# Kernel optimization log

Measured on AMD Instinct MI355X. Metric: run time of the kernel, lower is better.

Reference implementation:

```python
import jax, jax.numpy as jnp
import numpy as np

N = 50000      # nodes
E = 800000     # edges (avg degree 16)
D = 128        # extended_lat_size = latent_size(124) + 4
G = 256        # number of graphs in the batch
H = 8 * D      # 1024, hidden width of MLP stack


def _w(k, shape):
    return jax.random.normal(k, shape, jnp.float32) * 0.02


def setup_inputs() -> dict:
    key = jax.random.key(0)
    ks = jax.random.split(key, 20)
    x = jax.random.normal(ks[0], (N, D), jnp.float32)
    edge_index = jax.random.randint(ks[1], (2, E), 0, N, dtype=jnp.int32)
    batch_vector = jnp.sort(jax.random.randint(ks[2], (N,), 0, G, dtype=jnp.int32))
    return {
        "x": x,
        "edge_index": edge_index,
        "batch_vector": batch_vector,
        # GCNConv layers
        "W1": _w(ks[3], (D, 2 * D)), "b1": jnp.zeros((2 * D,), jnp.float32),
        "W2": _w(ks[4], (2 * D, D)), "b2": jnp.zeros((D,), jnp.float32),
        # lazy Linear stack (in-dims resolved from dataflow)
        "Wl1": _w(ks[5], (D, D)),   "bl1": jnp.zeros((D,), jnp.float32),
        "Wl2": _w(ks[6], (D, H)),   "bl2": jnp.zeros((H,), jnp.float32),
        "Wl22": _w(ks[7], (H, H)),  "bl22": jnp.zeros((H,), jnp.float32),
        "Wl23": _w(ks[8], (H, H)),  "bl23": jnp.zeros((H,), jnp.float32),
        "Wl3": _w(ks[9], (H, D)),   "bl3": jnp.zeros((D,), jnp.float32),
    }


def gcn_conv(x, W, b, row, col):
    """PyG GCNConv: linear transform, add self-loops, symmetric norm, scatter-add."""
    h = x @ W  # [N, F_out]
    n = x.shape[0]
    loop = jnp.arange(n, dtype=row.dtype)
    r = jnp.concatenate([row, loop])   # source nodes
    c = jnp.concatenate([col, loop])   # target nodes
    deg = jax.ops.segment_sum(jnp.ones_like(c, dtype=h.dtype), c, num_segments=n)
    dinv = jnp.where(deg > 0, jax.lax.rsqrt(deg), 0.0)
    norm = dinv[r] * dinv[c]                         # [E+N]
    msg = h[r] * norm[:, None]                       # gather + scale
    out = jax.ops.segment_sum(msg, c, num_segments=n)  # scatter-add
    return out + b


def global_mean_pool(x, batch, num_graphs):
    s = jax.ops.segment_sum(x, batch, num_segments=num_graphs)
    cnt = jax.ops.segment_sum(jnp.ones((x.shape[0],), x.dtype), batch, num_segments=num_graphs)
    return s / jnp.maximum(cnt, 1.0)[:, None]


def reference(x, edge_index, batch_vector, W1, b1, W2, b2,
              Wl1, bl1, Wl2, bl2, Wl22, bl22, Wl23, bl23, Wl3, bl3):
    row, col = edge_index[0], edge_index[1]
    h = jax.nn.relu(gcn_conv(x, W1, b1, row, col))
    h = jax.nn.relu(gcn_conv(h, W2, b2, row, col))
    g = global_mean_pool(h, batch_vector, G)         # [G, D]
    g = jax.nn.relu(g @ Wl1 + bl1)
    g = jax.nn.relu(g @ Wl2 + bl2)
    g = jax.nn.relu(g @ Wl22 + bl22)
    g = jax.nn.relu(g @ Wl23 + bl23)
    g = g @ Wl3 + bl3                                 # [G, D]
    return jnp.squeeze(g).reshape(-1)                 # flatten -> [G*D]
```

## Files before the change

kernel.cpp:

```cpp
#include <hip/hip_runtime.h>


typedef __attribute__((ext_vector_type(8))) short bf16x8;
typedef __attribute__((ext_vector_type(8))) ushort u16x8;
typedef __attribute__((ext_vector_type(4))) float f32x4;

#define ADJ_STRIDE 64

__device__ __forceinline__ ushort f2bf(float f) {
    unsigned u = __float_as_uint(f);
    unsigned r = (u + 0x7FFFu + ((u >> 16) & 1u)) >> 16;
    return (ushort)r;
}
__device__ __forceinline__ float bf2f(ushort h) {
    return __uint_as_float(((unsigned)h) << 16);
}
__device__ __forceinline__ float bflo(unsigned u) {
    return __uint_as_float(u << 16);
}
__device__ __forceinline__ float bfhi(unsigned u) {
    return __uint_as_float(u & 0xffff0000u);
}
__device__ __forceinline__ float idinv(int d) {
    return rsqrtf((float)(d + 1));
}
__device__ __forceinline__ void gload16(const ushort* g, ushort* l) {
    __builtin_amdgcn_global_load_lds(
        (const __attribute__((address_space(1))) void*)g,
        (__attribute__((address_space(3))) void*)l, 16, 0, 0);
}

#define SWZ(r) (((r) >> 1) & 3)

struct PreArgs {
    const int* row;
    const int* col;
    int E, N;
    int* indeg;
    int* adjf;
    const float* W[7];
    ushort* Th[7];
    ushort* Tl[7];
    int K[7], Nn[7], off[8];
    const float* x;
    ushort* xb;
    int total8;
    int nFill, nT;
};

__global__ __launch_bounds__(256) void preproc_mega_kernel(PreArgs a) {
    __shared__ float sm[64][65];
    int bid = blockIdx.x;
    int tid = threadIdx.x;

    if (bid < a.nFill) {
        int r = bid & 7, chunk = bid >> 3;
        int lo = (int)(((long long)a.N * r) >> 3);
        int hi = (int)(((long long)a.N * (r + 1)) >> 3);
        int E4 = a.E >> 2;
#pragma unroll
        for (int v = 0; v < 2; ++v) {
            int i = chunk * 512 + v * 256 + tid;
            if (i < E4) {
                int c0 = __builtin_nontemporal_load(a.col + i * 4 + 0);
                int c1 = __builtin_nontemporal_load(a.col + i * 4 + 1);
                int c2 = __builtin_nontemporal_load(a.col + i * 4 + 2);
                int c3 = __builtin_nontemporal_load(a.col + i * 4 + 3);
                int r0 = __builtin_nontemporal_load(a.row + i * 4 + 0);
                int r1 = __builtin_nontemporal_load(a.row + i * 4 + 1);
                int r2 = __builtin_nontemporal_load(a.row + i * 4 + 2);
                int r3 = __builtin_nontemporal_load(a.row + i * 4 + 3);
                if (c0 >= lo && c0 < hi) {
                    int p = atomicAdd(&a.indeg[c0], 1);
                    if (p < ADJ_STRIDE) a.adjf[(c0 << 6) + p] = r0;
                }
                if (c1 >= lo && c1 < hi) {
                    int p = atomicAdd(&a.indeg[c1], 1);
                    if (p < ADJ_STRIDE) a.adjf[(c1 << 6) + p] = r1;
                }
                if (c2 >= lo && c2 < hi) {
                    int p = atomicAdd(&a.indeg[c2], 1);
                    if (p < ADJ_STRIDE) a.adjf[(c2 << 6) + p] = r2;
                }
                if (c3 >= lo && c3 < hi) {
                    int p = atomicAdd(&a.indeg[c3], 1);
                    if (p < ADJ_STRIDE) a.adjf[(c3 << 6) + p] = r3;
                }
            }
        }
        if (bid == 0 && tid < (a.E & 3)) {
            int e = (a.E & ~3) + tid;
            int c = a.col[e];
            int p = atomicAdd(&a.indeg[c], 1);
            if (p < ADJ_STRIDE) a.adjf[(c << 6) + p] = a.row[e];
        }
        return;
    }

    if (bid < a.nFill + a.nT) {
        int b = bid - a.nFill;
        int j = 0;
#pragma unroll
        for (int t = 1; t < 7; ++t) if (b >= a.off[t]) j = t;
        int local = b - a.off[j];
        int K = a.K[j], Nn = a.Nn[j];
        int kt = K >> 6;
        int k0 = (local % kt) * 64, n0 = (local / kt) * 64;
        const float* W = a.W[j];
        ushort* Th = a.Th[j];
        ushort* Tl = a.Tl[j];

        int r = tid >> 2, cq = tid & 3;
#pragma unroll
        for (int i = 0; i < 4; ++i) {
            float4 v = *(const float4*)(W + (size_t)(k0 + r) * Nn + n0 + cq * 16 + i * 4);
            sm[r][cq * 16 + i * 4 + 0] = v.x;
            sm[r][cq * 16 + i * 4 + 1] = v.y;
            sm[r][cq * 16 + i * 4 + 2] = v.z;
            sm[r][cq * 16 + i * 4 + 3] = v.w;
        }
        __syncthreads();
        int n = tid >> 2, kq = tid & 3;
        ushort h[16], l[16];
#pragma unroll
        for (int i = 0; i < 16; ++i) {
            float v = sm[kq * 16 + i][n];
            h[i] = f2bf(v);
            l[i] = f2bf(v - bf2f(h[i]));
        }
        size_t o = (size_t)(n0 + n) * K + k0 + kq * 16;
        *(u16x8*)(&Th[o]) = *(u16x8*)&h[0];
        *(u16x8*)(&Th[o + 8]) = *(u16x8*)&h[8];
        *(u16x8*)(&Tl[o]) = *(u16x8*)&l[0];
        *(u16x8*)(&Tl[o + 8]) = *(u16x8*)&l[8];
        return;
    }

    {
        int idx = (bid - a.nFill - a.nT) * 256 + tid;
        if (idx >= a.total8) return;
        const float4* xp = (const float4*)a.x;
        float4 v0 = xp[idx * 2], v1 = xp[idx * 2 + 1];
        ushort h[8] = {f2bf(v0.x), f2bf(v0.y), f2bf(v0.z), f2bf(v0.w),
                       f2bf(v1.x), f2bf(v1.y), f2bf(v1.z), f2bf(v1.w)};
        *(u16x8*)(a.xb + (size_t)idx * 8) = *(u16x8*)&h[0];
    }
}

template<int MODE>
__global__ void aggregate_bf16_kernel(const ushort* __restrict__ hsb,
                                      const int* __restrict__ indeg,
                                      const int* __restrict__ adjf,
                                      const float* __restrict__ bias,
                                      float* __restrict__ outf,
                                      ushort* __restrict__ outh, ushort* __restrict__ outl,
                                      int N) {
    int wv = (blockIdx.x * blockDim.x + threadIdx.x) >> 6;
    int lane = threadIdx.x & 63;
    int half = lane >> 5, l32 = lane & 31;
    int node = wv * 2 + half;
    bool active = node < N;
    int nd = active ? node : N - 1;
    const uint2* base = (const uint2*)hsb;
    int degRaw = indeg[nd];
    float dself = idinv(degRaw);
    uint2 sa = base[(size_t)nd * 32 + l32];
    float sw = (MODE == 1) ? dself : 1.f;
    float ax = sw * bflo(sa.x), ay = sw * bfhi(sa.x);
    float az = sw * bflo(sa.y), aw = sw * bfhi(sa.y);
    int s = nd << 6;
    int deg = active ? min(degRaw, ADJ_STRIDE) : 0;
    int mx = max(deg, __shfl_xor(deg, 32));
    for (int j = 0; j < mx; j += 16) {
        int idx[16]; float wgt[16];
#pragma unroll
        for (int k = 0; k < 16; ++k) {
            int jj = j + k;
            bool valid = jj < deg;
            int ld = adjf[s + (valid ? jj : 0)];
            idx[k] = valid ? ld : 0;
            wgt[k] = valid ? 1.f : 0.f;
        }
        uint2 v[16];
#pragma unroll
        for (int k = 0; k < 16; ++k) v[k] = base[(size_t)idx[k] * 32 + l32];
        if (MODE == 1) {
#pragma unroll
            for (int k = 0; k < 16; ++k) wgt[k] *= idinv(indeg[idx[k]]);
        }
#pragma unroll
        for (int k = 0; k < 16; ++k) {
            ax = fmaf(wgt[k], bflo(v[k].x), ax);
            ay = fmaf(wgt[k], bfhi(v[k].x), ay);
            az = fmaf(wgt[k], bflo(v[k].y), az);
            aw = fmaf(wgt[k], bfhi(v[k].y), aw);
        }
    }
    ax *= dself; ay *= dself; az *= dself; aw *= dself;
    if (!active) return;
    if (MODE == 0) {
        float4 b = ((const float4*)bias)[l32];
        ax = fmaxf(ax + b.x, 0.f); ay = fmaxf(ay + b.y, 0.f);
        az = fmaxf(az + b.z, 0.f); aw = fmaxf(aw + b.w, 0.f);
        ((float4*)outf)[(size_t)node * 32 + l32] = make_float4(ax, ay, az, aw);
    } else {
        ushort h0 = f2bf(ax), h1 = f2bf(ay), h2 = f2bf(az), h3 = f2bf(aw);
        uint2 hv = make_uint2((unsigned)h0 | ((unsigned)h1 << 16),
                              (unsigned)h2 | ((unsigned)h3 << 16));
        ushort l0 = f2bf(ax - bf2f(h0)), l1 = f2bf(ay - bf2f(h1));
        ushort l2 = f2bf(az - bf2f(h2)), l3 = f2bf(aw - bf2f(h3));
        uint2 lv = make_uint2((unsigned)l0 | ((unsigned)l1 << 16),
                              (unsigned)l2 | ((unsigned)l3 << 16));
        ((uint2*)outh)[(size_t)node * 32 + l32] = hv;
        ((uint2*)outl)[(size_t)node * 32 + l32] = lv;
    }
}

__global__ __launch_bounds__(512) void gcn_mid_kernel(
        const ushort* __restrict__ Ah, const ushort* __restrict__ Al,
        const ushort* __restrict__ B1h, const ushort* __restrict__ B1l,
        const ushort* __restrict__ B2h, const ushort* __restrict__ B2l,
        const float* __restrict__ bias1, const int* __restrict__ indeg,
        ushort* __restrict__ outb, int M) {
    __shared__ __align__(16) ushort t1f[2 * 128 * 256 + 2 * 128 * 32];
    const int tid = threadIdx.x;
    const int w = tid >> 6, lane = tid & 63;
    const int bm = blockIdx.x * 128;
    const int sq = lane >> 4, r16 = lane & 15;

    {
        const int wr = w >> 2, wc = w & 3;
        f32x4 acc1[4][4];
#pragma unroll
        for (int i = 0; i < 4; ++i)
#pragma unroll
            for (int j = 0; j < 4; ++j) acc1[i][j] = (f32x4)0.f;

        for (int kk = 0; kk < 128; kk += 32) {
            {
                int rowi = w * 16 + (lane >> 2);
                int u = lane & 3;
                int colk = kk + 8 * (u ^ SWZ(rowi));
                gload16(Ah + (size_t)(bm + rowi) * 128 + colk, t1f + w * 512);
                gload16(Al + (size_t)(bm + rowi) * 128 + colk, t1f + 4096 + w * 512);
            }
#pragma unroll
            for (int v = 0; v < 2; ++v) {
                int chunk = v * 8 + w;
                int rowi = chunk * 16 + (lane >> 2);
                int u = lane & 3;
                int colk = kk + 8 * (u ^ SWZ(rowi));
                gload16(B1h + (size_t)rowi * 128 + colk, t1f + 8192 + chunk * 512);
                gload16(B1l + (size_t)rowi * 128 + colk, t1f + 16384 + chunk * 512);
            }
            __syncthreads();

            bf16x8 ah[4], al[4], bh[4], bl[4];
#pragma unroll
            for (int f = 0; f < 4; ++f) {
                int ra = wr * 64 + f * 16 + r16;
                int oa = ra * 32 + 8 * (sq ^ SWZ(ra));
                ah[f] = *(const bf16x8*)(t1f + oa);
                al[f] = *(const bf16x8*)(t1f + 4096 + oa);
                int rb = wc * 64 + f * 16 + r16;
                int ob = rb * 32 + 8 * (sq ^ SWZ(rb));
                bh[f] = *(const bf16x8*)(t1f + 8192 + ob);
                bl[f] = *(const bf16x8*)(t1f + 16384 + ob);
            }
#pragma unroll
            for (int i = 0; i < 4; ++i)
#pragma unroll
                for (int j = 0; j < 4; ++j) {
                    acc1[i][j] = __builtin_amdgcn_mfma_f32_16x16x32_bf16(ah[i], bh[j], acc1[i][j], 0, 0, 0);
                    acc1[i][j] = __builtin_amdgcn_mfma_f32_16x16x32_bf16(ah[i], bl[j], acc1[i][j], 0, 0, 0);
                    acc1[i][j] = __builtin_amdgcn_mfma_f32_16x16x32_bf16(al[i], bh[j], acc1[i][j], 0, 0, 0);
                }
            __syncthreads();
        }

        const int q4 = lane >> 4;
#pragma unroll
        for (int j = 0; j < 4; ++j) {
            int col = wc * 64 + j * 16 + r16;
            float bv = bias1[col];
            int cslot = col >> 3, coff = col & 7;
#pragma unroll
            for (int i = 0; i < 4; ++i) {
                int rowb = wr * 64 + i * 16 + q4 * 4;
#pragma unroll
                for (int r = 0; r < 4; ++r) {
                    int rowt = rowb + r;
                    float v = fmaxf(acc1[i][j][r] + bv, 0.f);
                    ushort h = f2bf(v);
                    ushort lo = f2bf(v - bf2f(h));
                    int a = rowt * 256 + (((cslot ^ (rowt & 7)) << 3) + coff);
                    t1f[a] = h;
                    t1f[32768 + a] = lo;
                }
            }
        }
    }

    {
        const int wr2 = w >> 1, wc2 = w & 1;
        const int q4 = lane >> 4;
        f32x4 acc2[2][4];
#pragma unroll
        for (int i = 0; i < 2; ++i)
#pragma unroll
            for (int j = 0; j < 4; ++j) acc2[i][j] = (f32x4)0.f;

        for (int kk = 0; kk < 256; kk += 32) {
            {
                int rowi = w * 16 + (lane >> 2);
                int u = lane & 3;
                int colk = kk + 8 * (u ^ SWZ(rowi));
                gload16(B2h + (size_t)rowi * 256 + colk, t1f + 65536 + w * 512);
                gload16(B2l + (size_t)rowi * 256 + colk, t1f + 69632 + w * 512);
            }
            __syncthreads();

            bf16x8 a2h[2], a2l[2], b2h[4], b2l[4];
#pragma unroll
            for (int f = 0; f < 2; ++f) {
                int ra = wr2 * 32 + f * 16 + r16;
                int k0 = kk + sq * 8;
                int ao = ra * 256 + (((k0 >> 3) ^ (ra & 7)) << 3);
                a2h[f] = *(const bf16x8*)(t1f + ao);
                a2l[f] = *(const bf16x8*)(t1f + 32768 + ao);
            }
#pragma unroll
            for (int f = 0; f < 4; ++f) {
                int rb = wc2 * 64 + f * 16 + r16;
                int ob = rb * 32 + 8 * (sq ^ SWZ(rb));
                b2h[f] = *(const bf16x8*)(t1f + 65536 + ob);
                b2l[f] = *(const bf16x8*)(t1f + 69632 + ob);
            }
#pragma unroll
            for (int i = 0; i < 2; ++i)
#pragma unroll
                for (int j = 0; j < 4; ++j) {
                    acc2[i][j] = __builtin_amdgcn_mfma_f32_16x16x32_bf16(a2h[i], b2h[j], acc2[i][j], 0, 0, 0);
                    acc2[i][j] = __builtin_amdgcn_mfma_f32_16x16x32_bf16(a2h[i], b2l[j], acc2[i][j], 0, 0, 0);
                    acc2[i][j] = __builtin_amdgcn_mfma_f32_16x16x32_bf16(a2l[i], b2h[j], acc2[i][j], 0, 0, 0);
                }
            __syncthreads();
        }

#pragma unroll
        for (int i = 0; i < 2; ++i) {
            int row0 = bm + wr2 * 32 + i * 16 + q4 * 4;
            if (row0 >= M) continue;
#pragma unroll
            for (int j = 0; j < 4; ++j) {
                int col = wc2 * 64 + j * 16 + r16;
#pragma unroll
                for (int r = 0; r < 4; ++r) {
                    float dv = idinv(indeg[row0 + r]);
                    outb[(size_t)(row0 + r) * 128 + col] =
                        f2bf(acc2[i][j][r] * dv);
                }
            }
        }
    }
}

template<int BM, int BN, int EPI>
__global__ __launch_bounds__(256) void gemm_bf16x3_kernel(
        const ushort* __restrict__ Ah, const ushort* __restrict__ Al,
        const ushort* __restrict__ Bth, const ushort* __restrict__ Btl,
        const float* __restrict__ bias,
        float* __restrict__ Cf, ushort* __restrict__ Ch, ushort* __restrict__ Cl,
        int M, int N, int K, int kChunk) {
    constexpr int WMm = BM / 2, WMn = BN / 2;
    constexpr int FRm = WMm / 16, FRn = WMn / 16;
    __shared__ __align__(16) ushort lds[(2 * BM + 2 * BN) * 32];
    const int tbB[4] = {0, BM * 64, 2 * BM * 64, (2 * BM + BN) * 64};

    const int tid = threadIdx.x;
    const int w = tid >> 6, lane = tid & 63;
    const int wr = w >> 1, wc = w & 1;
    const int bm = blockIdx.x * BM, bn = blockIdx.y * BN;
    const int k0 = blockIdx.z * kChunk;
    int k1 = k0 + kChunk; if (k1 > K) k1 = K;

    const ushort* srcs[4] = {
        Ah  + (size_t)bm * K, Al  + (size_t)bm * K,
        Bth + (size_t)bn * K, Btl + (size_t)bn * K };

    f32x4 acc[FRm][FRn];
#pragma unroll
    for (int i = 0; i < FRm; ++i)
#pragma unroll
        for (int j = 0; j < FRn; ++j) acc[i][j] = (f32x4)0.f;

    const int sq = lane >> 4, r16 = lane & 15;

    for (int kk = k0; kk < k1; kk += 32) {
#pragma unroll
        for (int t = 0; t < 4; ++t) {
            const int rows = (t < 2) ? BM : BN;
            const int nv = rows / 64;
#pragma unroll
            for (int v = 0; v < nv; ++v) {
                int chunk = v * 4 + w;
                int rowi = chunk * 16 + (lane >> 2);
                int u = lane & 3;
                int colk = kk + 8 * (u ^ SWZ(rowi));
                const ushort* g = srcs[t] + (size_t)rowi * K + colk;
                ushort* lp = (ushort*)((char*)lds + tbB[t] + chunk * 16 * 64);
                gload16(g, lp);
            }
        }
        __syncthreads();

        bf16x8 ah[FRm], al[FRm], bh[FRn], bl[FRn];
#pragma unroll
        for (int f = 0; f < FRm; ++f) {
            int ra = wr * WMm + f * 16 + r16;
            int oa = ra * 64 + 16 * (sq ^ SWZ(ra));
            ah[f] = *(const bf16x8*)((const char*)lds + tbB[0] + oa);
            al[f] = *(const bf16x8*)((const char*)lds + tbB[1] + oa);
        }
#pragma unroll
        for (int f = 0; f < FRn; ++f) {
            int rb = wc * WMn + f * 16 + r16;
            int ob = rb * 64 + 16 * (sq ^ SWZ(rb));
            bh[f] = *(const bf16x8*)((const char*)lds + tbB[2] + ob);
            bl[f] = *(const bf16x8*)((const char*)lds + tbB[3] + ob);
        }

#pragma unroll
        for (int i = 0; i < FRm; ++i)
#pragma unroll
            for (int j = 0; j < FRn; ++j) {
                acc[i][j] = __builtin_amdgcn_mfma_f32_16x16x32_bf16(ah[i], bh[j], acc[i][j], 0, 0, 0);
                acc[i][j] = __builtin_amdgcn_mfma_f32_16x16x32_bf16(ah[i], bl[j], acc[i][j], 0, 0, 0);
                acc[i][j] = __builtin_amdgcn_mfma_f32_16x16x32_bf16(al[i], bh[j], acc[i][j], 0, 0, 0);
            }
        __syncthreads();
    }

    const int q4 = lane >> 4;
#pragma unroll
    for (int i = 0; i < FRm; ++i) {
        int row0 = bm + wr * WMm + i * 16 + q4 * 4;
        if (row0 >= M) continue;
#pragma unroll
        for (int j = 0; j < FRn; ++j) {
            int colc = bn + wc * WMn + j * 16 + r16;
            if (EPI == 1) {
                float bv = bias[colc];
#pragma unroll
                for (int r = 0; r < 4; ++r) {
                    float v = fmaxf(acc[i][j][r] + bv, 0.f);
                    ushort h = f2bf(v);
                    ushort lo = f2bf(v - bf2f(h));
                    size_t o = (size_t)(row0 + r) * N + colc;
                    Ch[o] = h; Cl[o] = lo;
                }
            } else {
#pragma unroll
                for (int r = 0; r < 4; ++r)
                    atomicAdd(&Cf[(size_t)(row0 + r) * N + colc], acc[i][j][r]);
            }
        }
    }
}

__global__ void finish_kernel(const float* __restrict__ acc, const float* __restrict__ bias,
                              float* __restrict__ outf, ushort* __restrict__ outh,
                              ushort* __restrict__ outl, int total, int Ncols, int doRelu) {
    int idx = blockIdx.x * blockDim.x + threadIdx.x;
    if (idx >= total) return;
    float v = acc[idx] + bias[idx & (Ncols - 1)];
    if (doRelu) v = fmaxf(v, 0.f);
    if (outh) {
        ushort h = f2bf(v);
        outh[idx] = h;
        outl[idx] = f2bf(v - bf2f(h));
    } else {
        outf[idx] = v;
    }
}

__global__ void pool_kernel(const float* __restrict__ feats, const int* __restrict__ batch,
                            ushort* __restrict__ gh, ushort* __restrict__ gl, int N) {
    __shared__ float sm[256];
    int gid = blockIdx.x;
    int lo = 0, hi = N;
    while (lo < hi) { int m = (lo + hi) >> 1; if (batch[m] < gid) lo = m + 1; else hi = m; }
    int start = lo;
    lo = start; hi = N;
    while (lo < hi) { int m = (lo + hi) >> 1; if (batch[m] < gid + 1) lo = m + 1; else hi = m; }
    int end = lo;
    int tid = threadIdx.x;
    int f = tid & 127, half = tid >> 7;
    float acc = 0.f;
    for (int i = start + half; i < end; i += 2) acc += feats[(size_t)i * 128 + f];
    sm[tid] = acc;
    __syncthreads();
    if (half == 0) {
        acc += sm[tid + 128];
        int cnt = end - start; if (cnt < 1) cnt = 1;
        float m = acc / (float)cnt;
        ushort h = f2bf(m);
        gh[gid * 128 + f] = h;
        gl[gid * 128 + f] = f2bf(m - bf2f(h));
    }
}


extern "C" void kernel_launch(void* const* d_in, const int* in_sizes, int n_in,
                              void* d_out, int out_size, void* d_ws, size_t ws_size,
                              hipStream_t stream) {
    const float* x    = (const float*)d_in[0];
    const int*   ei   = (const int*)d_in[1];
    const int*   batch= (const int*)d_in[2];
    const float* W1   = (const float*)d_in[3];
    const float* b1   = (const float*)d_in[4];
    const float* W2   = (const float*)d_in[5];
    const float* b2   = (const float*)d_in[6];
    const float* Wl1  = (const float*)d_in[7];
    const float* bl1  = (const float*)d_in[8];
    const float* Wl2  = (const float*)d_in[9];
    const float* bl2  = (const float*)d_in[10];
    const float* Wl22 = (const float*)d_in[11];
    const float* bl22 = (const float*)d_in[12];
    const float* Wl23 = (const float*)d_in[13];
    const float* bl23 = (const float*)d_in[14];
    const float* Wl3  = (const float*)d_in[15];
    const float* bl3  = (const float*)d_in[16];

    const int D = 128;
    const int N = in_sizes[0] / D;
    const int E = in_sizes[1] / 2;
    const int G = out_size / D;
    const int H = in_sizes[10];
    const int Mpad = ((N + 127) / 128) * 128;
    const int* row = ei;
    const int* col = ei + E;
    float* out = (float*)d_out;

    char* ws = (char*)d_ws;
    auto alloc = [&](size_t bytes) -> void* {
        void* p = (void*)ws;
        ws += (bytes + 255) & ~(size_t)255;
        return p;
    };
    int*    indeg  = (int*)alloc((size_t)N * 4);
    float*  accb   = (float*)alloc((size_t)G * H * 4);
    float*  accb2  = (float*)alloc((size_t)G * H * 4);
    float*  accf   = (float*)alloc((size_t)G * 128 * 4);
    char*   zeroEnd = ws;
    int*    adjf   = (int*)alloc((size_t)N * ADJ_STRIDE * 4);
    ushort* W1th   = (ushort*)alloc((size_t)256 * 128 * 2);
    ushort* W1tl   = (ushort*)alloc((size_t)256 * 128 * 2);
    ushort* W2th   = (ushort*)alloc((size_t)128 * 256 * 2);
    ushort* W2tl   = (ushort*)alloc((size_t)128 * 256 * 2);
    ushort* Tl1h  = (ushort*)alloc((size_t)128 * 128 * 2);
    ushort* Tl1l  = (ushort*)alloc((size_t)128 * 128 * 2);
    ushort* Tl2h  = (ushort*)alloc((size_t)H * 128 * 2);
    ushort* Tl2l  = (ushort*)alloc((size_t)H * 128 * 2);
    ushort* Tl22h = (ushort*)alloc((size_t)H * H * 2);
    ushort* Tl22l = (ushort*)alloc((size_t)H * H * 2);
    ushort* Tl23h = (ushort*)alloc((size_t)H * H * 2);
    ushort* Tl23l = (ushort*)alloc((size_t)H * H * 2);
    ushort* Tl3h  = (ushort*)alloc((size_t)128 * H * 2);
    ushort* Tl3l  = (ushort*)alloc((size_t)128 * H * 2);
    ushort* xb     = (ushort*)alloc((size_t)Mpad * 128 * 2);
    ushort* yh     = (ushort*)alloc((size_t)Mpad * 128 * 2);
    ushort* yl     = (ushort*)alloc((size_t)Mpad * 128 * 2);
    ushort* hs2b   = (ushort*)alloc((size_t)Mpad * 128 * 2);
    float*  yf     = (float*)alloc((size_t)Mpad * 128 * 4);
    ushort* gh     = (ushort*)alloc((size_t)G * 128 * 2);
    ushort* gl     = (ushort*)alloc((size_t)G * 128 * 2);
    ushort* a1h    = (ushort*)alloc((size_t)G * 128 * 2);
    ushort* a1l    = (ushort*)alloc((size_t)G * 128 * 2);
    ushort* a2h    = (ushort*)alloc((size_t)G * H * 2);
    ushort* a2l    = (ushort*)alloc((size_t)G * H * 2);
    ushort* a3h    = (ushort*)alloc((size_t)G * H * 2);
    ushort* a3l    = (ushort*)alloc((size_t)G * H * 2);
    ushort* a4h    = (ushort*)alloc((size_t)G * H * 2);
    ushort* a4l    = (ushort*)alloc((size_t)G * H * 2);

    hipMemsetAsync(indeg, 0, (size_t)(zeroEnd - (char*)indeg), stream);

    const int CHUNKS = (E / 4 + 511) / 512;
    {
        PreArgs pa;
        pa.row = row; pa.col = col; pa.E = E; pa.N = N;
        pa.indeg = indeg; pa.adjf = adjf;
        const float* Ws[7]  = {W1, W2, Wl1, Wl2, Wl22, Wl23, Wl3};
        ushort* Ths[7]      = {W1th, W2th, Tl1h, Tl2h, Tl22h, Tl23h, Tl3h};
        ushort* Tls[7]      = {W1tl, W2tl, Tl1l, Tl2l, Tl22l, Tl23l, Tl3l};
        int Ks[7]           = {128, 256, 128, 128, H, H, H};
        int Nns[7]          = {256, 128, 128, H, H, H, 128};
        int off = 0;
        for (int j = 0; j < 7; ++j) {
            pa.W[j] = Ws[j]; pa.Th[j] = Ths[j]; pa.Tl[j] = Tls[j];
            pa.K[j] = Ks[j]; pa.Nn[j] = Nns[j];
            pa.off[j] = off;
            off += (Ks[j] / 64) * (Nns[j] / 64);
        }
        pa.off[7] = off;
        pa.x = x; pa.xb = xb; pa.total8 = N * 16;
        pa.nFill = 8 * CHUNKS;
        pa.nT = off;
        int nCvt = (pa.total8 + 255) / 256;
        preproc_mega_kernel<<<pa.nFill + pa.nT + nCvt, 256, 0, stream>>>(pa);
    }

    aggregate_bf16_kernel<1><<<(N + 7) / 8, 256, 0, stream>>>(
        xb, indeg, adjf, nullptr, nullptr, yh, yl, N);

    gcn_mid_kernel<<<Mpad / 128, 512, 0, stream>>>(
        yh, yl, W1th, W1tl, W2th, W2tl, b1, indeg, hs2b, N);

    aggregate_bf16_kernel<0><<<(N + 7) / 8, 256, 0, stream>>>(
        hs2b, indeg, adjf, b2, yf, nullptr, nullptr, N);

    pool_kernel<<<G, 256, 0, stream>>>(yf, batch, gh, gl, N);

    {
        dim3 grid(G / 64, 2);
        gemm_bf16x3_kernel<64, 64, 1><<<grid, 256, 0, stream>>>(
            gh, gl, Tl1h, Tl1l, bl1, nullptr, a1h, a1l, G, 128, 128, 128);
    }
    {
        dim3 grid(G / 64, H / 64);
        gemm_bf16x3_kernel<64, 64, 1><<<grid, 256, 0, stream>>>(
            a1h, a1l, Tl2h, Tl2l, bl2, nullptr, a2h, a2l, G, H, 128, 128);
    }
    {
        dim3 grid(G / 64, H / 64, 8);
        gemm_bf16x3_kernel<64, 64, 3><<<grid, 256, 0, stream>>>(
            a2h, a2l, Tl22h, Tl22l, nullptr, accb, nullptr, nullptr, G, H, H, 128);
        finish_kernel<<<(G * H + 255) / 256, 256, 0, stream>>>(
            accb, bl22, nullptr, a3h, a3l, G * H, H, 1);
    }
    {
        dim3 grid(G / 64, H / 64, 8);
        gemm_bf16x3_kernel<64, 64, 3><<<grid, 256, 0, stream>>>(
            a3h, a3l, Tl23h, Tl23l, nullptr, accb2, nullptr, nullptr, G, H, H, 128);
        finish_kernel<<<(G * H + 255) / 256, 256, 0, stream>>>(
            accb2, bl23, nullptr, a4h, a4l, G * H, H, 1);
    }
    {
        dim3 grid(G / 64, 2, 8);
        gemm_bf16x3_kernel<64, 64, 3><<<grid, 256, 0, stream>>>(
            a4h, a4l, Tl3h, Tl3l, nullptr, accf, nullptr, nullptr, G, 128, H, 128);
        finish_kernel<<<(G * 128 + 255) / 256, 256, 0, stream>>>(
            accf, bl3, out, nullptr, nullptr, G * 128, 128, 0);
    }
}
```

Baseline: 243.4 us.

## Fuse first aggregation into GCN GEMM kernel and store final features as bf16

```diff
diff --git a/kernel.cpp b/kernel.cpp
--- a/kernel.cpp
+++ b/kernel.cpp
@@ -147,14 +147,210 @@
     }
 }
 
-template<int MODE>
-__global__ void aggregate_bf16_kernel(const ushort* __restrict__ hsb,
-                                      const int* __restrict__ indeg,
-                                      const int* __restrict__ adjf,
-                                      const float* __restrict__ bias,
-                                      float* __restrict__ outf,
-                                      ushort* __restrict__ outh, ushort* __restrict__ outl,
-                                      int N) {
+__global__ __launch_bounds__(512) void gcn_fused_kernel(
+        const ushort* __restrict__ xb, const int* __restrict__ indeg,
+        const int* __restrict__ adjf,
+        const ushort* __restrict__ B1h, const ushort* __restrict__ B1l,
+        const ushort* __restrict__ B2h, const ushort* __restrict__ B2l,
+        const float* __restrict__ bias1,
+        ushort* __restrict__ outb, int M) {
+    __shared__ __align__(16) ushort t1f[2 * 128 * 256 + 2 * 128 * 32];
+    const int tid = threadIdx.x;
+    const int w = tid >> 6, lane = tid & 63;
+    const int bm = blockIdx.x * 128;
+    const int sq = lane >> 4, r16 = lane & 15;
+
+    {
+        const int half = lane >> 5, l32 = lane & 31;
+        const uint2* base = (const uint2*)xb;
+        const int t16 = l32 >> 1, hf = l32 & 1;
+#pragma unroll 1
+        for (int it = 0; it < 8; ++it) {
+            int r = it * 16 + w * 2 + half;
+            int node = bm + r;
+            int nd = (node < M) ? node : M - 1;
+            int degRaw = indeg[nd];
+            float dself = idinv(degRaw);
+            uint2 sa = base[(size_t)nd * 32 + l32];
+            float ax = dself * bflo(sa.x), ay = dself * bfhi(sa.x);
+            float az = dself * bflo(sa.y), aw = dself * bfhi(sa.y);
+            int s = nd << 6;
+            int deg = (node < M) ? min(degRaw, ADJ_STRIDE) : 0;
+            int mx = max(deg, __shfl_xor(deg, 32));
+            for (int j = 0; j < mx; j += 16) {
+                int idx[16]; float wgt[16];
+#pragma unroll
+                for (int k = 0; k < 16; ++k) {
+                    int jj = j + k;
+                    bool valid = jj < deg;
+                    int ld = adjf[s + (valid ? jj : 0)];
+                    idx[k] = valid ? ld : 0;
+                    wgt[k] = valid ? 1.f : 0.f;
+                }
+                uint2 v[16];
+#pragma unroll
+                for (int k = 0; k < 16; ++k) v[k] = base[(size_t)idx[k] * 32 + l32];
+#pragma unroll
+                for (int k = 0; k < 16; ++k) wgt[k] *= idinv(indeg[idx[k]]);
+#pragma unroll
+                for (int k = 0; k < 16; ++k) {
+                    ax = fmaf(wgt[k], bflo(v[k].x), ax);
+                    ay = fmaf(wgt[k], bfhi(v[k].x), ay);
+                    az = fmaf(wgt[k], bflo(v[k].y), az);
+                    aw = fmaf(wgt[k], bfhi(v[k].y), aw);
+                }
+            }
+            ax *= dself; ay *= dself; az *= dself; aw *= dself;
+            ushort h0 = f2bf(ax), h1 = f2bf(ay), h2 = f2bf(az), h3 = f2bf(aw);
+            uint2 hv = make_uint2((unsigned)h0 | ((unsigned)h1 << 16),
+                                  (unsigned)h2 | ((unsigned)h3 << 16));
+            ushort l0 = f2bf(ax - bf2f(h0)), l1 = f2bf(ay - bf2f(h1));
+            ushort l2 = f2bf(az - bf2f(h2)), l3 = f2bf(aw - bf2f(h3));
+            uint2 lv = make_uint2((unsigned)l0 | ((unsigned)l1 << 16),
+                                  (unsigned)l2 | ((unsigned)l3 << 16));
+            int aoff = r * 128 + ((t16 ^ (r & 7)) << 3) + hf * 4;
+            *(uint2*)(t1f + aoff) = hv;
+            *(uint2*)(t1f + 16384 + aoff) = lv;
+        }
+    }
+    __syncthreads();
+
+    {
+        const int wr = w >> 2, wc = w & 3;
+        f32x4 acc1[4][4];
+#pragma unroll
+        for (int i = 0; i < 4; ++i)
+#pragma unroll
+            for (int j = 0; j < 4; ++j) acc1[i][j] = (f32x4)0.f;
+
+        for (int kk = 0; kk < 128; kk += 32) {
+#pragma unroll
+            for (int v = 0; v < 2; ++v) {
+                int chunk = v * 8 + w;
+                int rowi = chunk * 16 + (lane >> 2);
+                int u = lane & 3;
+                int colk = kk + 8 * (u ^ SWZ(rowi));
+                gload16(B1h + (size_t)rowi * 128 + colk, t1f + 32768 + chunk * 512);
+                gload16(B1l + (size_t)rowi * 128 + colk, t1f + 40960 + chunk * 512);
+            }
+            __syncthreads();
+
+            bf16x8 ah[4], al[4], bh[4], bl[4];
+#pragma unroll
+            for (int f = 0; f < 4; ++f) {
+                int ra = wr * 64 + f * 16 + r16;
+                int k0 = kk + sq * 8;
+                int ao = ra * 128 + (((k0 >> 3) ^ (ra & 7)) << 3);
+                ah[f] = *(const bf16x8*)(t1f + ao);
+                al[f] = *(const bf16x8*)(t1f + 16384 + ao);
+                int rb = wc * 64 + f * 16 + r16;
+                int ob = rb * 32 + 8 * (sq ^ SWZ(rb));
+                bh[f] = *(const bf16x8*)(t1f + 32768 + ob);
+                bl[f] = *(const bf16x8*)(t1f + 40960 + ob);
+            }
+#pragma unroll
+            for (int i = 0; i < 4; ++i)
+#pragma unroll
+                for (int j = 0; j < 4; ++j) {
+                    acc1[i][j] = __builtin_amdgcn_mfma_f32_16x16x32_bf16(ah[i], bh[j], acc1[i][j], 0, 0, 0);
+                    acc1[i][j] = __builtin_amdgcn_mfma_f32_16x16x32_bf16(ah[i], bl[j], acc1[i][j], 0, 0, 0);
+                    acc1[i][j] = __builtin_amdgcn_mfma_f32_16x16x32_bf16(al[i], bh[j], acc1[i][j], 0, 0, 0);
+                }
+            __syncthreads();
+        }
+
+        const int q4 = lane >> 4;
+#pragma unroll
+        for (int j = 0; j < 4; ++j) {
+            int col = wc * 64 + j * 16 + r16;
+            float bv = bias1[col];
+            int cslot = col >> 3, coff = col & 7;
+#pragma unroll
+            for (int i = 0; i < 4; ++i) {
+                int rowb = wr * 64 + i * 16 + q4 * 4;
+#pragma unroll
+                for (int r = 0; r < 4; ++r) {
+                    int rowt = rowb + r;
+                    float v = fmaxf(acc1[i][j][r] + bv, 0.f);
+                    ushort h = f2bf(v);
+                    ushort lo = f2bf(v - bf2f(h));
+                    int a = rowt * 256 + (((cslot ^ (rowt & 7)) << 3) + coff);
+                    t1f[a] = h;
+                    t1f[32768 + a] = lo;
+                }
+            }
+        }
+    }
+
+    {
+        const int wr2 = w >> 1, wc2 = w & 1;
+        const int q4 = lane >> 4;
+        f32x4 acc2[2][4];
+#pragma unroll
+        for (int i = 0; i < 2; ++i)
+#pragma unroll
+            for (int j = 0; j < 4; ++j) acc2[i][j] = (f32x4)0.f;
+
+        for (int kk = 0; kk < 256; kk += 32) {
+            {
+                int rowi = w * 16 + (lane >> 2);
+                int u = lane & 3;
+                int colk = kk + 8 * (u ^ SWZ(rowi));
+                gload16(B2h + (size_t)rowi * 256 + colk, t1f + 65536 + w * 512);
+                gload16(B2l + (size_t)rowi * 256 + colk, t1f + 69632 + w * 512);
+            }
+            __syncthreads();
+
+            bf16x8 a2h[2], a2l[2], b2h[4], b2l[4];
+#pragma unroll
+            for (int f = 0; f < 2; ++f) {
+                int ra = wr2 * 32 + f * 16 + r16;
+                int k0 = kk + sq * 8;
+                int ao = ra * 256 + (((k0 >> 3) ^ (ra & 7)) << 3);
+                a2h[f] = *(const bf16x8*)(t1f + ao);
+                a2l[f] = *(const bf16x8*)(t1f + 32768 + ao);
+            }
+#pragma unroll
+            for (int f = 0; f < 4; ++f) {
+                int rb = wc2 * 64 + f * 16 + r16;
+                int ob = rb * 32 + 8 * (sq ^ SWZ(rb));
+                b2h[f] = *(const bf16x8*)(t1f + 65536 + ob);
+                b2l[f] = *(const bf16x8*)(t1f + 69632 + ob);
+            }
+#pragma unroll
+            for (int i = 0; i < 2; ++i)
+#pragma unroll
+                for (int j = 0; j < 4; ++j) {
+                    acc2[i][j] = __builtin_amdgcn_mfma_f32_16x16x32_bf16(a2h[i], b2h[j], acc2[i][j], 0, 0, 0);
+                    acc2[i][j] = __builtin_amdgcn_mfma_f32_16x16x32_bf16(a2h[i], b2l[j], acc2[i][j], 0, 0, 0);
+                    acc2[i][j] = __builtin_amdgcn_mfma_f32_16x16x32_bf16(a2l[i], b2h[j], acc2[i][j], 0, 0, 0);
+                }
+            __syncthreads();
+        }
+
+#pragma unroll
+        for (int i = 0; i < 2; ++i) {
+            int row0 = bm + wr2 * 32 + i * 16 + q4 * 4;
+            if (row0 >= M) continue;
+#pragma unroll
+            for (int j = 0; j < 4; ++j) {
+                int col = wc2 * 64 + j * 16 + r16;
+#pragma unroll
+                for (int r = 0; r < 4; ++r) {
+                    float dv = idinv(indeg[row0 + r]);
+                    outb[(size_t)(row0 + r) * 128 + col] =
+                        f2bf(acc2[i][j][r] * dv);
+                }
+            }
+        }
+    }
+}
+
+__global__ void aggregate2_kernel(const ushort* __restrict__ hsb,
+                                  const int* __restrict__ indeg,
+                                  const int* __restrict__ adjf,
+                                  const float* __restrict__ bias,
+                                  ushort* __restrict__ outb, int N) {
     int wv = (blockIdx.x * blockDim.x + threadIdx.x) >> 6;
     int lane = threadIdx.x & 63;
     int half = lane >> 5, l32 = lane & 31;
@@ -165,9 +361,8 @@
     int degRaw = indeg[nd];
     float dself = idinv(degRaw);
     uint2 sa = base[(size_t)nd * 32 + l32];
-    float sw = (MODE == 1) ? dself : 1.f;
-    float ax = sw * bflo(sa.x), ay = sw * bfhi(sa.x);
-    float az = sw * bflo(sa.y), aw = sw * bfhi(sa.y);
+    float ax = bflo(sa.x), ay = bfhi(sa.x);
+    float az = bflo(sa.y), aw = bfhi(sa.y);
     int s = nd << 6;
     int deg = active ? min(degRaw, ADJ_STRIDE) : 0;
     int mx = max(deg, __shfl_xor(deg, 32));
@@ -184,10 +379,6 @@
         uint2 v[16];
 #pragma unroll
         for (int k = 0; k < 16; ++k) v[k] = base[(size_t)idx[k] * 32 + l32];
-        if (MODE == 1) {
-#pragma unroll
-            for (int k = 0; k < 16; ++k) wgt[k] *= idinv(indeg[idx[k]]);
-        }
 #pragma unroll
         for (int k = 0; k < 16; ++k) {
             ax = fmaf(wgt[k], bflo(v[k].x), ax);
@@ -196,173 +387,16 @@
             aw = fmaf(wgt[k], bfhi(v[k].y), aw);
         }
     }
-    ax *= dself; ay *= dself; az *= dself; aw *= dself;
     if (!active) return;
-    if (MODE == 0) {
-        float4 b = ((const float4*)bias)[l32];
-        ax = fmaxf(ax + b.x, 0.f); ay = fmaxf(ay + b.y, 0.f);
-        az = fmaxf(az + b.z, 0.f); aw = fmaxf(aw + b.w, 0.f);
-        ((float4*)outf)[(size_t)node * 32 + l32] = make_float4(ax, ay, az, aw);
-    } else {
-        ushort h0 = f2bf(ax), h1 = f2bf(ay), h2 = f2bf(az), h3 = f2bf(aw);
-        uint2 hv = make_uint2((unsigned)h0 | ((unsigned)h1 << 16),
-                              (unsigned)h2 | ((unsigned)h3 << 16));
-        ushort l0 = f2bf(ax - bf2f(h0)), l1 = f2bf(ay - bf2f(h1));
-        ushort l2 = f2bf(az - bf2f(h2)), l3 = f2bf(aw - bf2f(h3));
-        uint2 lv = make_uint2((unsigned)l0 | ((unsigned)l1 << 16),
-                              (unsigned)l2 | ((unsigned)l3 << 16));
-        ((uint2*)outh)[(size_t)node * 32 + l32] = hv;
-        ((uint2*)outl)[(size_t)node * 32 + l32] = lv;
-    }
-}
-
-__global__ __launch_bounds__(512) void gcn_mid_kernel(
-        const ushort* __restrict__ Ah, const ushort* __restrict__ Al,
-        const ushort* __restrict__ B1h, const ushort* __restrict__ B1l,
-        const ushort* __restrict__ B2h, const ushort* __restrict__ B2l,
-        const float* __restrict__ bias1, const int* __restrict__ indeg,
-        ushort* __restrict__ outb, int M) {
-    __shared__ __align__(16) ushort t1f[2 * 128 * 256 + 2 * 128 * 32];
-    const int tid = threadIdx.x;
-    const int w = tid >> 6, lane = tid & 63;
-    const int bm = blockIdx.x * 128;
-    const int sq = lane >> 4, r16 = lane & 15;
-
-    {
-        const int wr = w >> 2, wc = w & 3;
-        f32x4 acc1[4][4];
-#pragma unroll
-        for (int i = 0; i < 4; ++i)
-#pragma unroll
-            for (int j = 0; j < 4; ++j) acc1[i][j] = (f32x4)0.f;
-
-        for (int kk = 0; kk < 128; kk += 32) {
-            {
-                int rowi = w * 16 + (lane >> 2);
-                int u = lane & 3;
-                int colk = kk + 8 * (u ^ SWZ(rowi));
-                gload16(Ah + (size_t)(bm + rowi) * 128 + colk, t1f + w * 512);
-                gload16(Al + (size_t)(bm + rowi) * 128 + colk, t1f + 4096 + w * 512);
-            }
-#pragma unroll
-            for (int v = 0; v < 2; ++v) {
-                int chunk = v * 8 + w;
-                int rowi = chunk * 16 + (lane >> 2);
-                int u = lane & 3;
-                int colk = kk + 8 * (u ^ SWZ(rowi));
-                gload16(B1h + (size_t)rowi * 128 + colk, t1f + 8192 + chunk * 512);
-                gload16(B1l + (size_t)rowi * 128 + colk, t1f + 16384 + chunk * 512);
-            }
-            __syncthreads();
-
-            bf16x8 ah[4], al[4], bh[4], bl[4];
-#pragma unroll
-            for (int f = 0; f < 4; ++f) {
-                int ra = wr * 64 + f * 16 + r16;
-                int oa = ra * 32 + 8 * (sq ^ SWZ(ra));
-                ah[f] = *(const bf16x8*)(t1f + oa);
-                al[f] = *(const bf16x8*)(t1f + 4096 + oa);
-                int rb = wc * 64 + f * 16 + r16;
-                int ob = rb * 32 + 8 * (sq ^ SWZ(rb));
-                bh[f] = *(const bf16x8*)(t1f + 8192 + ob);
-                bl[f] = *(const bf16x8*)(t1f + 16384 + ob);
-            }
-#pragma unroll
-            for (int i = 0; i < 4; ++i)
-#pragma unroll
-                for (int j = 0; j < 4; ++j) {
-                    acc1[i][j] = __builtin_amdgcn_mfma_f32_16x16x32_bf16(ah[i], bh[j], acc1[i][j], 0, 0, 0);
-                    acc1[i][j] = __builtin_amdgcn_mfma_f32_16x16x32_bf16(ah[i], bl[j], acc1[i][j], 0, 0, 0);
-                    acc1[i][j] = __builtin_amdgcn_mfma_f32_16x16x32_bf16(al[i], bh[j], acc1[i][j], 0, 0, 0);
-                }
-            __syncthreads();
-        }
-
-        const int q4 = lane >> 4;
-#pragma unroll
-        for (int j = 0; j < 4; ++j) {
-            int col = wc * 64 + j * 16 + r16;
-            float bv = bias1[col];
-            int cslot = col >> 3, coff = col & 7;
-#pragma unroll
-            for (int i = 0; i < 4; ++i) {
-                int rowb = wr * 64 + i * 16 + q4 * 4;
-#pragma unroll
-                for (int r = 0; r < 4; ++r) {
-                    int rowt = rowb + r;
-                    float v = fmaxf(acc1[i][j][r] + bv, 0.f);
-                    ushort h = f2bf(v);
-                    ushort lo = f2bf(v - bf2f(h));
-                    int a = rowt * 256 + (((cslot ^ (rowt & 7)) << 3) + coff);
-                    t1f[a] = h;
-                    t1f[32768 + a] = lo;
-                }
-            }
-        }
-    }
-
-    {
-        const int wr2 = w >> 1, wc2 = w & 1;
-        const int q4 = lane >> 4;
-        f32x4 acc2[2][4];
-#pragma unroll
-        for (int i = 0; i < 2; ++i)
-#pragma unroll
-            for (int j = 0; j < 4; ++j) acc2[i][j] = (f32x4)0.f;
-
-        for (int kk = 0; kk < 256; kk += 32) {
-            {
-                int rowi = w * 16 + (lane >> 2);
-                int u = lane & 3;
-                int colk = kk + 8 * (u ^ SWZ(rowi));
-                gload16(B2h + (size_t)rowi * 256 + colk, t1f + 65536 + w * 512);
-                gload16(B2l + (size_t)rowi * 256 + colk, t1f + 69632 + w * 512);
-            }
-            __syncthreads();
-
-            bf16x8 a2h[2], a2l[2], b2h[4], b2l[4];
-#pragma unroll
-            for (int f = 0; f < 2; ++f) {
-                int ra = wr2 * 32 + f * 16 + r16;
-                int k0 = kk + sq * 8;
-                int ao = ra * 256 + (((k0 >> 3) ^ (ra & 7)) << 3);
-                a2h[f] = *(const bf16x8*)(t1f + ao);
-                a2l[f] = *(const bf16x8*)(t1f + 32768 + ao);
-            }
-#pragma unroll
-            for (int f = 0; f < 4; ++f) {
-                int rb = wc2 * 64 + f * 16 + r16;
-                int ob = rb * 32 + 8 * (sq ^ SWZ(rb));
-                b2h[f] = *(const bf16x8*)(t1f + 65536 + ob);
-                b2l[f] = *(const bf16x8*)(t1f + 69632 + ob);
-            }
-#pragma unroll
-            for (int i = 0; i < 2; ++i)
-#pragma unroll
-                for (int j = 0; j < 4; ++j) {
-                    acc2[i][j] = __builtin_amdgcn_mfma_f32_16x16x32_bf16(a2h[i], b2h[j], acc2[i][j], 0, 0, 0);
-                    acc2[i][j] = __builtin_amdgcn_mfma_f32_16x16x32_bf16(a2h[i], b2l[j], acc2[i][j], 0, 0, 0);
-                    acc2[i][j] = __builtin_amdgcn_mfma_f32_16x16x32_bf16(a2l[i], b2h[j], acc2[i][j], 0, 0, 0);
-                }
-            __syncthreads();
-        }
-
-#pragma unroll
-        for (int i = 0; i < 2; ++i) {
-            int row0 = bm + wr2 * 32 + i * 16 + q4 * 4;
-            if (row0 >= M) continue;
-#pragma unroll
-            for (int j = 0; j < 4; ++j) {
-                int col = wc2 * 64 + j * 16 + r16;
-#pragma unroll
-                for (int r = 0; r < 4; ++r) {
-                    float dv = idinv(indeg[row0 + r]);
-                    outb[(size_t)(row0 + r) * 128 + col] =
-                        f2bf(acc2[i][j][r] * dv);
-                }
-            }
-        }
-    }
+    float4 b = ((const float4*)bias)[l32];
+    ax = fmaxf(fmaf(ax, dself, b.x), 0.f);
+    ay = fmaxf(fmaf(ay, dself, b.y), 0.f);
+    az = fmaxf(fmaf(az, dself, b.z), 0.f);
+    aw = fmaxf(fmaf(aw, dself, b.w), 0.f);
+    ushort h0 = f2bf(ax), h1 = f2bf(ay), h2 = f2bf(az), h3 = f2bf(aw);
+    uint2 hv = make_uint2((unsigned)h0 | ((unsigned)h1 << 16),
+                          (unsigned)h2 | ((unsigned)h3 << 16));
+    ((uint2*)outb)[(size_t)node * 32 + l32] = hv;
 }
 
 template<int BM, int BN, int EPI>
@@ -484,7 +518,7 @@
     }
 }
 
-__global__ void pool_kernel(const float* __restrict__ feats, const int* __restrict__ batch,
+__global__ void pool_kernel(const ushort* __restrict__ feats, const int* __restrict__ batch,
                             ushort* __restrict__ gh, ushort* __restrict__ gl, int N) {
     __shared__ float sm[256];
     int gid = blockIdx.x;
@@ -497,7 +531,7 @@
     int tid = threadIdx.x;
     int f = tid & 127, half = tid >> 7;
     float acc = 0.f;
-    for (int i = start + half; i < end; i += 2) acc += feats[(size_t)i * 128 + f];
+    for (int i = start + half; i < end; i += 2) acc += bf2f(feats[(size_t)i * 128 + f]);
     sm[tid] = acc;
     __syncthreads();
     if (half == 0) {
@@ -569,10 +603,8 @@
     ushort* Tl3h  = (ushort*)alloc((size_t)128 * H * 2);
     ushort* Tl3l  = (ushort*)alloc((size_t)128 * H * 2);
     ushort* xb     = (ushort*)alloc((size_t)Mpad * 128 * 2);
-    ushort* yh     = (ushort*)alloc((size_t)Mpad * 128 * 2);
-    ushort* yl     = (ushort*)alloc((size_t)Mpad * 128 * 2);
     ushort* hs2b   = (ushort*)alloc((size_t)Mpad * 128 * 2);
-    float*  yf     = (float*)alloc((size_t)Mpad * 128 * 4);
+    ushort* yfb    = (ushort*)alloc((size_t)Mpad * 128 * 2);
     ushort* gh     = (ushort*)alloc((size_t)G * 128 * 2);
     ushort* gl     = (ushort*)alloc((size_t)G * 128 * 2);
     ushort* a1h    = (ushort*)alloc((size_t)G * 128 * 2);
@@ -611,16 +643,13 @@
         preproc_mega_kernel<<<pa.nFill + pa.nT + nCvt, 256, 0, stream>>>(pa);
     }
 
-    aggregate_bf16_kernel<1><<<(N + 7) / 8, 256, 0, stream>>>(
-        xb, indeg, adjf, nullptr, nullptr, yh, yl, N);
-
-    gcn_mid_kernel<<<Mpad / 128, 512, 0, stream>>>(
-        yh, yl, W1th, W1tl, W2th, W2tl, b1, indeg, hs2b, N);
-
-    aggregate_bf16_kernel<0><<<(N + 7) / 8, 256, 0, stream>>>(
-        hs2b, indeg, adjf, b2, yf, nullptr, nullptr, N);
-
-    pool_kernel<<<G, 256, 0, stream>>>(yf, batch, gh, gl, N);
+    gcn_fused_kernel<<<Mpad / 128, 512, 0, stream>>>(
+        xb, indeg, adjf, W1th, W1tl, W2th, W2tl, b1, hs2b, N);
+
+    aggregate2_kernel<<<(N + 7) / 8, 256, 0, stream>>>(
+        hs2b, indeg, adjf, b2, yfb, N);
+
+    pool_kernel<<<G, 256, 0, stream>>>(yfb, batch, gh, gl, N);
 
     {
         dim3 grid(G / 64, 2);
```

Measured after the change: 266.0 us. 9.3% more time.
